# Optimization experiments

Hardware: AMD Instinct MI355X
Metric: run time of the kernel (lower is better)

## Reference

```python
import jax, jax.numpy as jnp
import numpy as np

EPS_NORM = 1e-12   # F.normalize eps
EPS_PERP = 1e-10   # perplexity log eps
COMMIT = 0.25


def _l2norm(x):
    # matches F.normalize(p=2, dim=1) with eps clamp
    n = jnp.sqrt(jnp.sum(x * x, axis=1, keepdims=True))
    return x / jnp.maximum(n, EPS_NORM)


def setup_inputs() -> dict:
    key = jax.random.key(0)
    k1, k2 = jax.random.split(key)
    B, D, L, K = 8, 256, 4096, 4096
    inputs = jax.random.normal(k1, (B, D, L), dtype=jnp.float32)
    # nn.Embedding init uniform(-1/K, 1/K); use uniform at that scale
    weight = jax.random.uniform(k2, (K, D), minval=-1.0 / K, maxval=1.0 / K, dtype=jnp.float32)
    return {"inputs": inputs, "weight": weight}


def reference(inputs, weight):
    K, D = weight.shape
    x = jnp.transpose(inputs, (0, 2, 1))          # [B, L, D]
    flat = x.reshape(-1, D)                       # [N, D]
    N = flat.shape[0]
    sim = _l2norm(flat) @ _l2norm(weight).T       # [N, K] cosine similarity
    # argmin(1 - sim) == argmax(sim)
    idx = jnp.argmax(sim, axis=1)                 # [N]
    # one-hot @ weight is just a gather of the selected code rows
    quantized = weight[idx].reshape(x.shape)      # [B, L, D]
    e_latent = jnp.mean((jax.lax.stop_gradient(quantized) - x) ** 2)
    q_latent = jnp.mean((quantized - jax.lax.stop_gradient(x)) ** 2)
    loss = q_latent + COMMIT * e_latent
    # straight-through estimator
    q_st = x + jax.lax.stop_gradient(quantized - x)
    # avg_probs = mean of one-hot encodings = normalized histogram of idx
    counts = jnp.zeros((K,), dtype=jnp.float32).at[idx].add(1.0)
    avg_probs = counts / N
    perplexity = jnp.exp(-jnp.sum(avg_probs * jnp.log(avg_probs + EPS_PERP)))
    return jnp.transpose(q_st, (0, 2, 1)), loss, perplexity
```

## Files before the change

### kernel.cpp

```cpp
#include <hip/hip_runtime.h>
#include <stdint.h>

#define Bb 8
#define Dd 256
#define Ll 4096
#define Kk 4096
#define Nn (Bb * Ll)
#define OUT0 (Bb * Dd * Ll)

typedef int    int4v   __attribute__((ext_vector_type(4)));
typedef int    int8v   __attribute__((ext_vector_type(8)));
typedef float  floatx4 __attribute__((ext_vector_type(4)));

#define SCALE1 0x7F7F7F7F

union V8 { int8v v; int4v h[2]; };

__device__ __forceinline__ void async_load16(const void* g, void* l) {
    __builtin_amdgcn_global_load_lds((const __attribute__((address_space(1))) void*)g,
                                     (__attribute__((address_space(3))) void*)l, 16, 0, 0);
}

__global__ void k_prep(const float* __restrict__ w, unsigned char* __restrict__ wn,
                       int* __restrict__ counts) {
    int blk = blockIdx.x, tid = threadIdx.x;
    if (blk == 0)
        for (int i = tid; i < Kk + 2; i += 256) counts[i] = 0;
    int row  = blk * 4 + (tid >> 6);
    int lane = tid & 63;
    float4 v = ((const float4*)(w + (size_t)row * Dd))[lane];
    float ss = v.x*v.x + v.y*v.y + v.z*v.z + v.w*v.w;
#pragma unroll
    for (int m = 1; m < 64; m <<= 1) ss += __shfl_xor(ss, m, 64);
    float s = 16.0f / fmaxf(sqrtf(ss), 1e-12f);
    int p = __builtin_amdgcn_cvt_pk_fp8_f32(v.x * s, v.y * s, 0, false);
    p     = __builtin_amdgcn_cvt_pk_fp8_f32(v.z * s, v.w * s, p, true);
    ((int*)(wn + (size_t)row * Dd))[lane] = p;
}

__global__ __launch_bounds__(256, 3) void k_gemm_fused(
        const float* __restrict__ x, const unsigned char* __restrict__ Wn,
        const float* __restrict__ w, float* __restrict__ out,
        int* __restrict__ counts) {
    __shared__ __align__(16) unsigned char As[64 * 256];
    __shared__ __align__(16) unsigned char Bs[2][64 * 256];
    unsigned int (*red)[4] = (unsigned int (*)[4])(void*)As;
    int*   kidx  = (int*)(void*)(As + 1024);
    float* wsum  = (float*)(void*)(As + 1280);
    int*   lastp = (int*)(void*)(As + 1296);

    float* lossacc = (float*)(counts + Kk);
    int*   done    = counts + Kk + 1;

    int bid = blockIdx.x;
    int bm = ((bid & 7) << 6) | (bid >> 3);
    int tid = threadIdx.x, lane = tid & 63, wv = tid >> 6;
    int l15 = lane & 15, l4 = lane >> 4;

    int goff[4], loff[4];
#pragma unroll
    for (int j = 0; j < 4; ++j) {
        int q = j * 256 + tid;
        int col = q >> 4, p = q & 15;
        goff[j] = col * 256 + ((p ^ (col & 15)) << 4);
        loff[j] = q * 16;
    }

#pragma unroll
    for (int j = 0; j < 4; ++j)
        async_load16(Wn + goff[j], (unsigned char*)Bs[0] + loff[j]);

    int b = bm >> 6, l0 = (bm & 63) * 64;
    const float* xs = x + (size_t)b * Dd * Ll + l0;
    int lg = tid & 15, dgr = tid >> 4;
#pragma unroll
    for (int i = 0; i < 4; ++i) {
        int d0 = dgr * 4 + i * 64;
        const float* s0 = xs + (size_t)d0 * Ll + lg * 4;
        float4 f0 = *(const float4*)(s0);
        float4 f1 = *(const float4*)(s0 + Ll);
        float4 f2 = *(const float4*)(s0 + 2 * (size_t)Ll);
        float4 f3 = *(const float4*)(s0 + 3 * (size_t)Ll);
#pragma unroll
        for (int jl = 0; jl < 4; ++jl) {
            float a0 = ((const float*)&f0)[jl], a1 = ((const float*)&f1)[jl];
            float a2 = ((const float*)&f2)[jl], a3 = ((const float*)&f3)[jl];
            int pk = __builtin_amdgcn_cvt_pk_fp8_f32(a0, a1, 0, false);
            pk     = __builtin_amdgcn_cvt_pk_fp8_f32(a2, a3, pk, true);
            int l = lg * 4 + jl;
            *(int*)(As + l * 256 + (((d0 >> 4) ^ (l & 15)) << 4) + (d0 & 15)) = pk;
        }
    }
    __syncthreads();

    int8v af[4][2];
#pragma unroll
    for (int fm = 0; fm < 4; ++fm)
#pragma unroll
        for (int ks = 0; ks < 2; ++ks) {
            int l = fm * 16 + l15;
            int ch = ks * 8 + l4 * 2;
            V8 u;
            u.h[0] = *(const int4v*)(As + l * 256 + ((ch ^ l15) << 4));
            u.h[1] = *(const int4v*)(As + l * 256 + (((ch + 1) ^ l15) << 4));
            af[fm][ks] = u.v;
        }

    unsigned int rk[4][4];
#pragma unroll
    for (int fm = 0; fm < 4; ++fm)
#pragma unroll
        for (int r = 0; r < 4; ++r) rk[fm][r] = 0u;

    for (int cb = 0; cb < 64; ++cb) {
        if (cb < 63) {
            const unsigned char* g = Wn + (size_t)(cb + 1) * (64 * 256);
            unsigned char* lb = (unsigned char*)Bs[(cb + 1) & 1];
#pragma unroll
            for (int j = 0; j < 4; ++j)
                async_load16(g + goff[j], lb + loff[j]);
        }
        const unsigned char* bb = (const unsigned char*)Bs[cb & 1];
        int8v bf[2];
#pragma unroll
        for (int ks = 0; ks < 2; ++ks) {
            int col = wv * 16 + l15;
            int ch = ks * 8 + l4 * 2;
            V8 u;
            u.h[0] = *(const int4v*)(bb + col * 256 + ((ch ^ l15) << 4));
            u.h[1] = *(const int4v*)(bb + col * 256 + (((ch + 1) ^ l15) << 4));
            bf[ks] = u.v;
        }
        __builtin_amdgcn_s_setprio(1);
        floatx4 acc[4];
#pragma unroll
        for (int fm = 0; fm < 4; ++fm) {
            floatx4 a = (floatx4)512.0f;
            a = __builtin_amdgcn_mfma_scale_f32_16x16x128_f8f6f4(
                    af[fm][0], bf[0], a, 0, 0, 0, SCALE1, 0, SCALE1);
            a = __builtin_amdgcn_mfma_scale_f32_16x16x128_f8f6f4(
                    af[fm][1], bf[1], a, 0, 0, 0, SCALE1, 0, SCALE1);
            acc[fm] = a;
        }
        __builtin_amdgcn_s_setprio(0);
        unsigned int i0 = (unsigned)(cb * 64 + wv * 16 + l15);
#pragma unroll
        for (int fm = 0; fm < 4; ++fm)
#pragma unroll
            for (int r = 0; r < 4; ++r) {
                unsigned int k0 = (__float_as_uint(acc[fm][r]) & 0xFFFFF000u) | i0;
                rk[fm][r] = rk[fm][r] > k0 ? rk[fm][r] : k0;
            }
        __syncthreads();
    }

#pragma unroll
    for (int fm = 0; fm < 4; ++fm)
#pragma unroll
        for (int r = 0; r < 4; ++r) {
            unsigned int kx = rk[fm][r];
#pragma unroll
            for (int md = 1; md <= 8; md <<= 1) {
                unsigned int o = (unsigned int)__shfl_xor((int)kx, md, 64);
                kx = kx > o ? kx : o;
            }
            if (l15 == 0) red[fm * 16 + l4 * 4 + r][wv] = kx;
        }
    __syncthreads();
    if (tid < 64) {
        unsigned int k0 = red[tid][0], k1 = red[tid][1];
        unsigned int k2 = red[tid][2], k3 = red[tid][3];
        unsigned int kx = k0 > k1 ? k0 : k1;
        kx = kx > k2 ? kx : k2;
        kx = kx > k3 ? kx : k3;
        int ix = (int)(kx & 0xFFFu);
        kidx[tid] = ix;
        atomicAdd(&counts[ix], 1);
    }
    __syncthreads();

    float ls = 0.f;
    {
        float* os = out + (size_t)b * Dd * Ll + l0;
        int r0 = lg * 4;
#pragma unroll
        for (int i = 0; i < 4; ++i) {
            int d0 = dgr * 4 + i * 64;
            float4 xv[4];
#pragma unroll
            for (int dd = 0; dd < 4; ++dd)
                xv[dd] = *(const float4*)(xs + (size_t)(d0 + dd) * Ll + lg * 4);
            float4 q4[4];
#pragma unroll
            for (int jl = 0; jl < 4; ++jl)
                q4[jl] = *(const float4*)(w + (size_t)kidx[r0 + jl] * Dd + d0);
#pragma unroll
            for (int dd = 0; dd < 4; ++dd) {
                float4 qq;
                qq.x = ((const float*)&q4[0])[dd];
                qq.y = ((const float*)&q4[1])[dd];
                qq.z = ((const float*)&q4[2])[dd];
                qq.w = ((const float*)&q4[3])[dd];
                float e0 = qq.x - xv[dd].x, e1 = qq.y - xv[dd].y;
                float e2 = qq.z - xv[dd].z, e3 = qq.w - xv[dd].w;
                ls += e0*e0 + e1*e1 + e2*e2 + e3*e3;
                *(float4*)(os + (size_t)(d0 + dd) * Ll + lg * 4) = qq;
            }
        }
    }

#pragma unroll
    for (int m = 1; m < 64; m <<= 1) ls += __shfl_xor(ls, m, 64);
    if (lane == 0) wsum[wv] = ls;
    __syncthreads();
    if (tid == 0) {
        atomicAdd(lossacc, wsum[0] + wsum[1] + wsum[2] + wsum[3]);
        __threadfence();
        *lastp = (atomicAdd(done, 1) == 511);
    }
    __syncthreads();
    if (*lastp) {
        __threadfence();
        float s = 0.f;
        for (int i = tid; i < Kk; i += 256) {
            float p = (float)counts[i] * (1.0f / Nn);
            s += p * logf(p + 1e-10f);
        }
#pragma unroll
        for (int m = 1; m < 64; m <<= 1) s += __shfl_xor(s, m, 64);
        if (lane == 0) wsum[wv] = s;
        __syncthreads();
        if (tid == 0) {
            out[OUT0]     = lossacc[0] * 1.25f / (float)OUT0;
            out[OUT0 + 1] = expf(-(wsum[0] + wsum[1] + wsum[2] + wsum[3]));
        }
    }
}

extern "C" void kernel_launch(void* const* d_in, const int* in_sizes, int n_in,
                              void* d_out, int out_size, void* d_ws, size_t ws_size,
                              hipStream_t stream) {
    const float* x = (const float*)d_in[0];
    const float* w = (const float*)d_in[1];
    float* out = (float*)d_out;
    char* ws = (char*)d_ws;

    unsigned char* wn     = (unsigned char*)ws;
    int*           counts = (int*)(ws + (1u << 20));

    k_prep      <<<1024, 256, 0, stream>>>(w, wn, counts);
    k_gemm_fused<<<512,  256, 0, stream>>>(x, wn, w, out, counts);
}
```

Baseline: 172.6 us.

## Give each wave a private triple-buffered codebook stream and drop block barriers

Each wave now loads only its own 16-column slice of the codebook into a per-wave triple buffer, using explicit vmcnt waits in place of the per-iteration __syncthreads. This is meant to remove block-wide barrier stalls in the main loop and let waves run out of step with each other, with prefetch two tiles ahead. Shared memory grows from 48KB to 64KB plus separate reduction arrays, so launch bounds drop from 3 to 2 blocks per CU, which lowers occupancy.

```diff
diff --git a/kernel.cpp b/kernel.cpp
--- a/kernel.cpp
+++ b/kernel.cpp
@@ -38,16 +38,16 @@
     ((int*)(wn + (size_t)row * Dd))[lane] = p;
 }
 
-__global__ __launch_bounds__(256, 3) void k_gemm_fused(
+__global__ __launch_bounds__(256, 2) void k_gemm_fused(
         const float* __restrict__ x, const unsigned char* __restrict__ Wn,
         const float* __restrict__ w, float* __restrict__ out,
         int* __restrict__ counts) {
     __shared__ __align__(16) unsigned char As[64 * 256];
-    __shared__ __align__(16) unsigned char Bs[2][64 * 256];
-    unsigned int (*red)[4] = (unsigned int (*)[4])(void*)As;
-    int*   kidx  = (int*)(void*)(As + 1024);
-    float* wsum  = (float*)(void*)(As + 1280);
-    int*   lastp = (int*)(void*)(As + 1296);
+    __shared__ __align__(16) unsigned char Bs[4][3][16 * 256];
+    __shared__ unsigned int red[64][4];
+    __shared__ int kidx[64];
+    __shared__ float wsum[4];
+    __shared__ int lastp;
 
     float* lossacc = (float*)(counts + Kk);
     int*   done    = counts + Kk + 1;
@@ -60,15 +60,19 @@
     int goff[4], loff[4];
 #pragma unroll
     for (int j = 0; j < 4; ++j) {
-        int q = j * 256 + tid;
-        int col = q >> 4, p = q & 15;
-        goff[j] = col * 256 + ((p ^ (col & 15)) << 4);
-        loff[j] = q * 16;
+        int c = j * 4 + l4;
+        goff[j] = c * 256 + ((l15 ^ (c & 15)) << 4);
+        loff[j] = j * 1024 + lane * 16;
     }
 
 #pragma unroll
     for (int j = 0; j < 4; ++j)
-        async_load16(Wn + goff[j], (unsigned char*)Bs[0] + loff[j]);
+        async_load16(Wn + (size_t)(0 * 4 + wv) * 4096 + goff[j],
+                     Bs[wv][0] + loff[j]);
+#pragma unroll
+    for (int j = 0; j < 4; ++j)
+        async_load16(Wn + (size_t)(1 * 4 + wv) * 4096 + goff[j],
+                     Bs[wv][1] + loff[j]);
 
     int b = bm >> 6, l0 = (bm & 63) * 64;
     const float* xs = x + (size_t)b * Dd * Ll + l0;
@@ -112,38 +116,37 @@
 #pragma unroll
         for (int r = 0; r < 4; ++r) rk[fm][r] = 0u;
 
-    for (int cb = 0; cb < 64; ++cb) {
-        if (cb < 63) {
-            const unsigned char* g = Wn + (size_t)(cb + 1) * (64 * 256);
-            unsigned char* lb = (unsigned char*)Bs[(cb + 1) & 1];
+    int base0 = l15 * 256;
+    for (int t = 0; t < 64; ++t) {
+        const unsigned char* p0 = Bs[wv][t % 3];
+        unsigned char*       p2 = Bs[wv][(t + 2) % 3];
+        if (t == 63) asm volatile("s_waitcnt vmcnt(0)" ::: "memory");
+        else         asm volatile("s_waitcnt vmcnt(4)" ::: "memory");
+        __builtin_amdgcn_sched_barrier(0);
+        if (t < 62) {
+            const unsigned char* g = Wn + (size_t)((t + 2) * 4 + wv) * 4096;
 #pragma unroll
             for (int j = 0; j < 4; ++j)
-                async_load16(g + goff[j], lb + loff[j]);
-        }
-        const unsigned char* bb = (const unsigned char*)Bs[cb & 1];
-        int8v bf[2];
-#pragma unroll
-        for (int ks = 0; ks < 2; ++ks) {
-            int col = wv * 16 + l15;
-            int ch = ks * 8 + l4 * 2;
-            V8 u;
-            u.h[0] = *(const int4v*)(bb + col * 256 + ((ch ^ l15) << 4));
-            u.h[1] = *(const int4v*)(bb + col * 256 + (((ch + 1) ^ l15) << 4));
-            bf[ks] = u.v;
-        }
+                async_load16(g + goff[j], p2 + loff[j]);
+        }
+        V8 bf0, bf1;
+        bf0.h[0] = *(const int4v*)(p0 + base0 + (((l4 * 2 + 0) ^ l15) << 4));
+        bf0.h[1] = *(const int4v*)(p0 + base0 + (((l4 * 2 + 1) ^ l15) << 4));
+        bf1.h[0] = *(const int4v*)(p0 + base0 + (((8 + l4 * 2 + 0) ^ l15) << 4));
+        bf1.h[1] = *(const int4v*)(p0 + base0 + (((8 + l4 * 2 + 1) ^ l15) << 4));
         __builtin_amdgcn_s_setprio(1);
         floatx4 acc[4];
 #pragma unroll
         for (int fm = 0; fm < 4; ++fm) {
             floatx4 a = (floatx4)512.0f;
             a = __builtin_amdgcn_mfma_scale_f32_16x16x128_f8f6f4(
-                    af[fm][0], bf[0], a, 0, 0, 0, SCALE1, 0, SCALE1);
+                    af[fm][0], bf0.v, a, 0, 0, 0, SCALE1, 0, SCALE1);
             a = __builtin_amdgcn_mfma_scale_f32_16x16x128_f8f6f4(
-                    af[fm][1], bf[1], a, 0, 0, 0, SCALE1, 0, SCALE1);
+                    af[fm][1], bf1.v, a, 0, 0, 0, SCALE1, 0, SCALE1);
             acc[fm] = a;
         }
         __builtin_amdgcn_s_setprio(0);
-        unsigned int i0 = (unsigned)(cb * 64 + wv * 16 + l15);
+        unsigned int i0 = (unsigned)((t * 4 + wv) * 16 + l15);
 #pragma unroll
         for (int fm = 0; fm < 4; ++fm)
 #pragma unroll
@@ -151,7 +154,6 @@
                 unsigned int k0 = (__float_as_uint(acc[fm][r]) & 0xFFFFF000u) | i0;
                 rk[fm][r] = rk[fm][r] > k0 ? rk[fm][r] : k0;
             }
-        __syncthreads();
     }
 
 #pragma unroll
@@ -216,10 +218,10 @@
     if (tid == 0) {
         atomicAdd(lossacc, wsum[0] + wsum[1] + wsum[2] + wsum[3]);
         __threadfence();
-        *lastp = (atomicAdd(done, 1) == 511);
-    }
-    __syncthreads();
-    if (*lastp) {
+        lastp = (atomicAdd(done, 1) == 511);
+    }
+    __syncthreads();
+    if (lastp) {
         __threadfence();
         float s = 0.f;
         for (int i = tid; i < Kk; i += 256) {
```

Result: faster. 168.5 us (-2.4%).
